# Kernel tuning notes

Measured on AMD Instinct MI355X. Metric: run time of the kernel, lower is better.

The kernel has to match this reference:

```python
import jax, jax.numpy as jnp
import numpy as np

N_NODES = 8192
N_EDGES = 16384
IN_CH = 32
HID = 64
OUT_CH = 2
EDGE_DIM = 4
N_LAYERS = 3
N_GRAPHS = 256
BN_EPS = 1e-5


def setup_inputs() -> dict:
    key = jax.random.key(0)
    ks = jax.random.split(key, 16)
    x = jax.random.normal(ks[0], (N_NODES, IN_CH), dtype=jnp.float32)
    edge_index = jax.random.randint(ks[1], (2, N_EDGES), 0, N_NODES, dtype=jnp.int32)
    edge_attr = jax.random.uniform(ks[2], (N_EDGES, EDGE_DIM), dtype=jnp.float32)
    batch = jnp.sort(jax.random.randint(ks[3], (N_NODES,), 0, N_GRAPHS, dtype=jnp.int32))
    s = 0.05
    params = {
        'lin_in_W': jax.random.normal(ks[4], (IN_CH, HID), jnp.float32) * s,
        'lin_in_b': jnp.zeros((HID,), jnp.float32),
        'edge_W': jax.random.normal(ks[5], (N_LAYERS, EDGE_DIM, HID * HID), jnp.float32) * s,
        'edge_b': jax.random.normal(ks[6], (N_LAYERS, HID * HID), jnp.float32) * s,
        'root_W': jax.random.normal(ks[7], (N_LAYERS, HID, HID), jnp.float32) * s,
        'conv_b': jnp.zeros((N_LAYERS, HID), jnp.float32),
        'bn_gamma': jnp.ones((N_LAYERS, HID), jnp.float32),
        'bn_beta': jnp.zeros((N_LAYERS, HID), jnp.float32),
        'bn_mean': jax.random.normal(ks[8], (N_LAYERS, HID), jnp.float32) * s,
        'bn_var': jax.random.uniform(ks[9], (N_LAYERS, HID), jnp.float32, 0.5, 1.5),
        'clf_W': jax.random.normal(ks[10], (HID, OUT_CH), jnp.float32) * s,
        'clf_b': jnp.zeros((OUT_CH,), jnp.float32),
    }
    return {'x': x, 'edge_index': edge_index, 'edge_attr': edge_attr, 'batch': batch, **params}


def reference(x, edge_index, edge_attr, batch, lin_in_W, lin_in_b, edge_W, edge_b,
              root_W, conv_b, bn_gamma, bn_beta, bn_mean, bn_var, clf_W, clf_b):
    # lin_in
    h = x @ lin_in_W + lin_in_b  # [N, H]
    src, dst = edge_index[0], edge_index[1]  # PyG: row0 = source j, row1 = target i
    for l in range(N_LAYERS):
        # edge network: per-edge weight matrix [E, H, H]
        W_e = (edge_attr @ edge_W[l] + edge_b[l]).reshape(N_EDGES, HID, HID)
        # message: gather x_j, per-edge matmul
        msg = jnp.einsum('eh,eho->eo', h[src], W_e)  # [E, H]
        # scatter-add aggregation at target nodes
        agg = jax.ops.segment_sum(msg, dst, num_segments=N_NODES)  # [N, H]
        # NNConv update: root transform + bias
        h = agg + h @ root_W[l] + conv_b[l]
        # BatchNorm1d (inference: running stats), then ReLU (dropout off in eval)
        h = (h - bn_mean[l]) * jax.lax.rsqrt(bn_var[l] + BN_EPS) * bn_gamma[l] + bn_beta[l]
        h = jax.nn.relu(h)
    # global_add_pool over graph ids
    pooled = jax.ops.segment_sum(h, batch, num_segments=N_GRAPHS)  # [G, H]
    return pooled @ clf_W + clf_b  # [G, OUT_CH]
```

## Files before the change

kernel.cpp:

```cpp
#include <hip/hip_runtime.h>
#include <hip/hip_bf16.h>

#define N_NODES 8192
#define N_EDGES 16384
#define IN_CH 32
#define HID 64
#define OUT_CH 2
#define EDGE_DIM 4
#define N_LAYERS 3
#define N_GRAPHS 256
#define BN_EPS 1e-5f
#define NT 512
#define NPB 32

__device__ __forceinline__ void ynet_phase(const float* __restrict__ hs,
                                           const float* __restrict__ eW,
                                           const float* __restrict__ eB,
                                           float4* __restrict__ y4,
                                           float* __restrict__ yb,
                                           int node0, int c, int g) {
    float acc[4][5];
#pragma unroll
    for (int j = 0; j < 4; ++j)
#pragma unroll
        for (int d = 0; d < 5; ++d) acc[j][d] = 0.f;

    const float4* h0v = (const float4*)(hs + (g * 4 + 0) * HID);
    const float4* h1v = (const float4*)(hs + (g * 4 + 1) * HID);
    const float4* h2v = (const float4*)(hs + (g * 4 + 2) * HID);
    const float4* h3v = (const float4*)(hs + (g * 4 + 3) * HID);

#pragma unroll 2
    for (int k4 = 0; k4 < HID / 4; ++k4) {
        float4 hv[4];
        hv[0] = h0v[k4]; hv[1] = h1v[k4]; hv[2] = h2v[k4]; hv[3] = h3v[k4];
        const float* hf = (const float*)hv;
#pragma unroll
        for (int kk = 0; kk < 4; ++kk) {
            int k = k4 * 4 + kk;
            float w0 = eW[0 * 4096 + k * 64 + c];
            float w1 = eW[1 * 4096 + k * 64 + c];
            float w2 = eW[2 * 4096 + k * 64 + c];
            float w3 = eW[3 * 4096 + k * 64 + c];
            float w4 = eB[k * 64 + c];
#pragma unroll
            for (int j = 0; j < 4; ++j) {
                float hk = hf[j * 4 + kk];
                acc[j][0] += hk * w0;
                acc[j][1] += hk * w1;
                acc[j][2] += hk * w2;
                acc[j][3] += hk * w3;
                acc[j][4] += hk * w4;
            }
        }
    }
#pragma unroll
    for (int j = 0; j < 4; ++j) {
        int n = node0 + g * 4 + j;
        y4[n * HID + c] = make_float4(acc[j][0], acc[j][1], acc[j][2], acc[j][3]);
        yb[n * HID + c] = acc[j][4];
    }
}

__global__ __launch_bounds__(NT) void k0_fused(
        const float* __restrict__ x,
        const float* __restrict__ Win, const float* __restrict__ bin,
        const float* __restrict__ eW0, const float* __restrict__ eB0,
        float* __restrict__ hA, float4* __restrict__ y4, float* __restrict__ yb,
        float* __restrict__ agg, float* __restrict__ pooled) {
    __shared__ float Wis[IN_CH * HID];
    __shared__ float xs[NPB * IN_CH];
    __shared__ float hs[NPB * HID];
    int t = threadIdx.x;
    int node0 = blockIdx.x * NPB;

    for (int i = t; i < NPB * HID; i += NT) agg[node0 * HID + i] = 0.f;
    if (t < 64) pooled[blockIdx.x * 64 + t] = 0.f;
    for (int i = t; i < IN_CH * HID; i += NT) Wis[i] = Win[i];
    for (int i = t; i < NPB * IN_CH; i += NT) xs[i] = x[node0 * IN_CH + i];
    __syncthreads();

    int c = t & 63, g = t >> 6;
    float b = bin[c];
    float a0 = b, a1 = b, a2 = b, a3 = b;
    const float* x0 = xs + (g * 4 + 0) * IN_CH;
    const float* x1 = xs + (g * 4 + 1) * IN_CH;
    const float* x2 = xs + (g * 4 + 2) * IN_CH;
    const float* x3 = xs + (g * 4 + 3) * IN_CH;
#pragma unroll
    for (int k = 0; k < IN_CH; ++k) {
        float wk = Wis[k * HID + c];
        a0 += x0[k] * wk; a1 += x1[k] * wk; a2 += x2[k] * wk; a3 += x3[k] * wk;
    }
    hs[(g * 4 + 0) * HID + c] = a0; hA[(node0 + g * 4 + 0) * HID + c] = a0;
    hs[(g * 4 + 1) * HID + c] = a1; hA[(node0 + g * 4 + 1) * HID + c] = a1;
    hs[(g * 4 + 2) * HID + c] = a2; hA[(node0 + g * 4 + 2) * HID + c] = a2;
    hs[(g * 4 + 3) * HID + c] = a3; hA[(node0 + g * 4 + 3) * HID + c] = a3;
    __syncthreads();

    ynet_phase(hs, eW0, eB0, y4, yb, node0, c, g);
}

__global__ __launch_bounds__(256) void edge_kernel(
        const float4* __restrict__ y4, const float* __restrict__ yb,
        const float* __restrict__ edge_attr, const int* __restrict__ edge_index,
        float* __restrict__ agg) {
    int e = blockIdx.x * 4 + (threadIdx.x >> 6);
    int lane = threadIdx.x & 63;
    int src = edge_index[e];
    int dst = edge_index[N_EDGES + e];
    float4 a = *(const float4*)(edge_attr + (size_t)e * 4);
    float4 yv = y4[(size_t)src * HID + lane];
    float m = a.x * yv.x + a.y * yv.y + a.z * yv.z + a.w * yv.w +
              yb[(size_t)src * HID + lane];
    atomicAdd(&agg[dst * HID + lane], m);
}

__global__ __launch_bounds__(NT) void k_upd_ynet(
        const float* __restrict__ h_in, float* __restrict__ agg,
        const float* __restrict__ rootW, const float* __restrict__ conv_b,
        const float* __restrict__ gam, const float* __restrict__ bet,
        const float* __restrict__ mu, const float* __restrict__ var,
        const float* __restrict__ eW_next, const float* __restrict__ eB_next,
        float* __restrict__ h_out, float4* __restrict__ y4, float* __restrict__ yb) {
    __shared__ float Ws[HID * HID];
    __shared__ float hsin[NPB * HID];
    __shared__ float hs[NPB * HID];
    int t = threadIdx.x;
    int node0 = blockIdx.x * NPB;
    for (int i = t; i < HID * HID; i += NT) Ws[i] = rootW[i];
    for (int i = t; i < NPB * HID; i += NT) hsin[i] = h_in[node0 * HID + i];
    __syncthreads();

    int c = t & 63, g = t >> 6;
    float scale = gam[c] * rsqrtf(var[c] + BN_EPS);
    float shift = bet[c] - mu[c] * scale;
    float cb = conv_b[c];

    float acc[4] = {0.f, 0.f, 0.f, 0.f};
    const float4* h0v = (const float4*)(hsin + (g * 4 + 0) * HID);
    const float4* h1v = (const float4*)(hsin + (g * 4 + 1) * HID);
    const float4* h2v = (const float4*)(hsin + (g * 4 + 2) * HID);
    const float4* h3v = (const float4*)(hsin + (g * 4 + 3) * HID);
#pragma unroll 4
    for (int k4 = 0; k4 < HID / 4; ++k4) {
        float4 hv[4];
        hv[0] = h0v[k4]; hv[1] = h1v[k4]; hv[2] = h2v[k4]; hv[3] = h3v[k4];
        const float* hf = (const float*)hv;
#pragma unroll
        for (int kk = 0; kk < 4; ++kk) {
            float wk = Ws[(k4 * 4 + kk) * 64 + c];
#pragma unroll
            for (int j = 0; j < 4; ++j) acc[j] += hf[j * 4 + kk] * wk;
        }
    }
#pragma unroll
    for (int j = 0; j < 4; ++j) {
        int node = node0 + g * 4 + j;
        float av = agg[node * HID + c];
        agg[node * HID + c] = 0.f;
        float v = fmaxf((av + acc[j] + cb) * scale + shift, 0.f);
        hs[(g * 4 + j) * HID + c] = v;
        h_out[node * HID + c] = v;
    }
    __syncthreads();

    ynet_phase(hs, eW_next, eB_next, y4, yb, node0, c, g);
}

__global__ __launch_bounds__(NT) void k_upd_pool(
        const float* __restrict__ h_in, float* __restrict__ agg,
        const float* __restrict__ rootW, const float* __restrict__ conv_b,
        const float* __restrict__ gam, const float* __restrict__ bet,
        const float* __restrict__ mu, const float* __restrict__ var,
        const int* __restrict__ batch, float* __restrict__ pooled) {
    __shared__ float Ws[HID * HID];
    __shared__ float hsin[NPB * HID];
    int t = threadIdx.x;
    int node0 = blockIdx.x * NPB;
    for (int i = t; i < HID * HID; i += NT) Ws[i] = rootW[i];
    for (int i = t; i < NPB * HID; i += NT) hsin[i] = h_in[node0 * HID + i];
    __syncthreads();

    int c = t & 63, g = t >> 6;
    float scale = gam[c] * rsqrtf(var[c] + BN_EPS);
    float shift = bet[c] - mu[c] * scale;
    float cb = conv_b[c];

    float acc[4] = {0.f, 0.f, 0.f, 0.f};
    const float4* h0v = (const float4*)(hsin + (g * 4 + 0) * HID);
    const float4* h1v = (const float4*)(hsin + (g * 4 + 1) * HID);
    const float4* h2v = (const float4*)(hsin + (g * 4 + 2) * HID);
    const float4* h3v = (const float4*)(hsin + (g * 4 + 3) * HID);
#pragma unroll 4
    for (int k4 = 0; k4 < HID / 4; ++k4) {
        float4 hv[4];
        hv[0] = h0v[k4]; hv[1] = h1v[k4]; hv[2] = h2v[k4]; hv[3] = h3v[k4];
        const float* hf = (const float*)hv;
#pragma unroll
        for (int kk = 0; kk < 4; ++kk) {
            float wk = Ws[(k4 * 4 + kk) * 64 + c];
#pragma unroll
            for (int j = 0; j < 4; ++j) acc[j] += hf[j * 4 + kk] * wk;
        }
    }
#pragma unroll
    for (int j = 0; j < 4; ++j) {
        int node = node0 + g * 4 + j;
        float av = agg[node * HID + c];
        agg[node * HID + c] = 0.f;
        float v = fmaxf((av + acc[j] + cb) * scale + shift, 0.f);
        atomicAdd(&pooled[batch[node] * HID + c], v);
    }
}

__global__ void clf_kernel(float* __restrict__ pooled,
                           const float* __restrict__ W,
                           const float* __restrict__ b,
                           float* __restrict__ out) {
    int gph = threadIdx.x;
    float acc0 = b[0], acc1 = b[1];
    float* pr = pooled + gph * HID;
#pragma unroll
    for (int k = 0; k < HID; ++k) {
        float p = pr[k];
        acc0 += p * W[k * 2 + 0];
        acc1 += p * W[k * 2 + 1];
    }
    out[gph * 2 + 0] = acc0;
    out[gph * 2 + 1] = acc1;
#pragma unroll
    for (int k = 0; k < HID; ++k) pr[k] = 0.f;
}

extern "C" void kernel_launch(void* const* d_in, const int* in_sizes, int n_in,
                              void* d_out, int out_size, void* d_ws, size_t ws_size,
                              hipStream_t stream) {
    const float* x         = (const float*)d_in[0];
    const int*   edge_index= (const int*)  d_in[1];
    const float* edge_attr = (const float*)d_in[2];
    const int*   batch     = (const int*)  d_in[3];
    const float* lin_in_W  = (const float*)d_in[4];
    const float* lin_in_b  = (const float*)d_in[5];
    const float* edge_W    = (const float*)d_in[6];
    const float* edge_b    = (const float*)d_in[7];
    const float* root_W    = (const float*)d_in[8];
    const float* conv_b    = (const float*)d_in[9];
    const float* bn_gamma  = (const float*)d_in[10];
    const float* bn_beta   = (const float*)d_in[11];
    const float* bn_mean   = (const float*)d_in[12];
    const float* bn_var    = (const float*)d_in[13];
    const float* clf_W     = (const float*)d_in[14];
    const float* clf_b     = (const float*)d_in[15];
    float* out = (float*)d_out;

    char* ws = (char*)d_ws;
    float*  hA     = (float*) (ws);
    float*  hB     = (float*) (ws + (size_t)2 * 1024 * 1024);
    float*  agg    = (float*) (ws + (size_t)4 * 1024 * 1024);
    float*  yb     = (float*) (ws + (size_t)6 * 1024 * 1024);
    float*  pooled = (float*) (ws + (size_t)8 * 1024 * 1024);
    float4* y4     = (float4*)(ws + (size_t)9 * 1024 * 1024);

    k0_fused<<<N_NODES / NPB, NT, 0, stream>>>(
        x, lin_in_W, lin_in_b, edge_W, edge_b, hA, y4, yb, agg, pooled);

    edge_kernel<<<N_EDGES / 4, 256, 0, stream>>>(y4, yb, edge_attr, edge_index, agg);

    k_upd_ynet<<<N_NODES / NPB, NT, 0, stream>>>(
        hA, agg, root_W, conv_b, bn_gamma, bn_beta, bn_mean, bn_var,
        edge_W + (size_t)1 * EDGE_DIM * HID * HID, edge_b + (size_t)1 * HID * HID,
        hB, y4, yb);

    edge_kernel<<<N_EDGES / 4, 256, 0, stream>>>(y4, yb, edge_attr, edge_index, agg);

    k_upd_ynet<<<N_NODES / NPB, NT, 0, stream>>>(
        hB, agg, root_W + (size_t)1 * HID * HID, conv_b + (size_t)1 * HID,
        bn_gamma + HID, bn_beta + HID, bn_mean + HID, bn_var + HID,
        edge_W + (size_t)2 * EDGE_DIM * HID * HID, edge_b + (size_t)2 * HID * HID,
        hA, y4, yb);

    edge_kernel<<<N_EDGES / 4, 256, 0, stream>>>(y4, yb, edge_attr, edge_index, agg);

    k_upd_pool<<<N_NODES / NPB, NT, 0, stream>>>(
        hA, agg, root_W + (size_t)2 * HID * HID, conv_b + (size_t)2 * HID,
        bn_gamma + 2 * HID, bn_beta + 2 * HID, bn_mean + 2 * HID, bn_var + 2 * HID,
        batch, pooled);

    clf_kernel<<<1, 256, 0, stream>>>(pooled, clf_W, clf_b, out);
}
```

Baseline: 89.86 us.

## Fuse all layers into one cooperative kernel with per-block edge gather

```diff
diff --git a/kernel.cpp b/kernel.cpp
--- a/kernel.cpp
+++ b/kernel.cpp
@@ -1,5 +1,7 @@
 #include <hip/hip_runtime.h>
-#include <hip/hip_bf16.h>
+#include <hip/hip_cooperative_groups.h>
+
+namespace cg = cooperative_groups;
 
 #define N_NODES 8192
 #define N_EDGES 16384
@@ -10,8 +12,23 @@
 #define N_LAYERS 3
 #define N_GRAPHS 256
 #define BN_EPS 1e-5f
+
+#define NBLK 256
 #define NT 512
 #define NPB 32
+#define CAP 24
+
+#define FB_NT 512
+#define FB_NPB 32
+
+struct KP {
+    const float* x; const int* edge_index; const float* edge_attr; const int* batch;
+    const float* lin_in_W; const float* lin_in_b; const float* edge_W; const float* edge_b;
+    const float* root_W; const float* conv_b; const float* bn_gamma; const float* bn_beta;
+    const float* bn_mean; const float* bn_var; const float* clf_W; const float* clf_b;
+    float* out;
+    float* y4A; float* ybA; float* y4B; float* ybB; float* pooled;
+};
 
 __device__ __forceinline__ void ynet_phase(const float* __restrict__ hs,
                                            const float* __restrict__ eW,
@@ -56,28 +73,159 @@
     }
 #pragma unroll
     for (int j = 0; j < 4; ++j) {
-        int n = node0 + g * 4 + j;
+        size_t n = node0 + g * 4 + j;
         y4[n * HID + c] = make_float4(acc[j][0], acc[j][1], acc[j][2], acc[j][3]);
         yb[n * HID + c] = acc[j][4];
     }
 }
 
-__global__ __launch_bounds__(NT) void k0_fused(
+__global__ __launch_bounds__(NT, 2) void mega(KP P) {
+    cg::grid_group grid = cg::this_grid();
+
+    __shared__ float  hs[NPB * HID];
+    __shared__ float  smem[HID * HID];
+    __shared__ int    cntL[NPB];
+    __shared__ int    esrcL[NPB * CAP];
+    __shared__ float4 ea4L[NPB * CAP];
+
+    const int t = threadIdx.x;
+    const int b = blockIdx.x;
+    const int node0 = b * NPB;
+    const int c = t & 63, g = t >> 6;
+
+    {
+        int gi = b * NT + t;
+        if (gi < N_GRAPHS * HID) P.pooled[gi] = 0.f;
+    }
+    if (t < NPB) cntL[t] = 0;
+    float* Wis = smem;
+    float* xs  = smem + IN_CH * HID;
+    for (int i = t; i < IN_CH * HID; i += NT) Wis[i] = P.lin_in_W[i];
+    for (int i = t; i < NPB * IN_CH; i += NT) xs[i] = P.x[node0 * IN_CH + i];
+    __syncthreads();
+
+    for (int e = t; e < N_EDGES; e += NT) {
+        int dst = P.edge_index[N_EDGES + e];
+        int local = dst - node0;
+        if ((unsigned)local < NPB) {
+            int slot = atomicAdd(&cntL[local], 1);
+            if (slot < CAP) {
+                esrcL[local * CAP + slot] = P.edge_index[e];
+                ea4L[local * CAP + slot] = *(const float4*)(P.edge_attr + 4 * (size_t)e);
+            }
+        }
+    }
+
+    {
+        float bb = P.lin_in_b[c];
+        float a0 = bb, a1 = bb, a2 = bb, a3 = bb;
+        const float* x0 = xs + (g * 4 + 0) * IN_CH;
+        const float* x1 = xs + (g * 4 + 1) * IN_CH;
+        const float* x2 = xs + (g * 4 + 2) * IN_CH;
+        const float* x3 = xs + (g * 4 + 3) * IN_CH;
+#pragma unroll
+        for (int k = 0; k < IN_CH; ++k) {
+            float wk = Wis[k * HID + c];
+            a0 += x0[k] * wk; a1 += x1[k] * wk; a2 += x2[k] * wk; a3 += x3[k] * wk;
+        }
+        hs[(g * 4 + 0) * HID + c] = a0;
+        hs[(g * 4 + 1) * HID + c] = a1;
+        hs[(g * 4 + 2) * HID + c] = a2;
+        hs[(g * 4 + 3) * HID + c] = a3;
+    }
+
+    ynet_phase(hs, P.edge_W, P.edge_b, (float4*)P.y4A, P.ybA, node0, c, g);
+
+    grid.sync();
+
+    const float4* ycur4 = (const float4*)P.y4A;
+    const float*  ycurb = P.ybA;
+    float4* ynxt4 = (float4*)P.y4B;
+    float*  ynxtb = P.ybB;
+
+    for (int l = 0; l < N_LAYERS; ++l) {
+        for (int i = t; i < HID * HID; i += NT)
+            smem[i] = P.root_W[(size_t)l * HID * HID + i];
+        __syncthreads();
+
+        float scale = P.bn_gamma[l * HID + c] * rsqrtf(P.bn_var[l * HID + c] + BN_EPS);
+        float shift = P.bn_beta[l * HID + c] - P.bn_mean[l * HID + c] * scale;
+        float cb = P.conv_b[l * HID + c];
+
+        float hnew[4];
+#pragma unroll
+        for (int j = 0; j < 4; ++j) {
+            int ln = g * 4 + j;
+            float m = 0.f;
+            int d = cntL[ln]; d = (d > CAP) ? CAP : d;
+            for (int s = 0; s < d; ++s) {
+                int src = esrcL[ln * CAP + s];
+                float4 a = ea4L[ln * CAP + s];
+                float4 yv = ycur4[(size_t)src * HID + c];
+                m += a.x * yv.x + a.y * yv.y + a.z * yv.z + a.w * yv.w +
+                     ycurb[(size_t)src * HID + c];
+            }
+            float acc = 0.f;
+            const float4* hv = (const float4*)(hs + ln * HID);
+#pragma unroll
+            for (int k4 = 0; k4 < HID / 4; ++k4) {
+                float4 h4 = hv[k4];
+                const float* hf = (const float*)&h4;
+#pragma unroll
+                for (int kk = 0; kk < 4; ++kk)
+                    acc += hf[kk] * smem[(k4 * 4 + kk) * HID + c];
+            }
+            hnew[j] = fmaxf((m + acc + cb) * scale + shift, 0.f);
+        }
+#pragma unroll
+        for (int j = 0; j < 4; ++j) hs[(g * 4 + j) * HID + c] = hnew[j];
+
+        if (l < N_LAYERS - 1) {
+            ynet_phase(hs, P.edge_W + (size_t)(l + 1) * EDGE_DIM * HID * HID,
+                       P.edge_b + (size_t)(l + 1) * HID * HID, ynxt4, ynxtb, node0, c, g);
+        } else {
+#pragma unroll
+            for (int j = 0; j < 4; ++j) {
+                int n = node0 + g * 4 + j;
+                atomicAdd(&P.pooled[P.batch[n] * HID + c], hnew[j]);
+            }
+        }
+        const float4* t4 = ycur4; ycur4 = (const float4*)ynxt4; ynxt4 = (float4*)t4;
+        const float*  tb = ycurb; ycurb = ynxtb; ynxtb = (float*)tb;
+
+        grid.sync();
+    }
+
+    if (b == 0 && t < N_GRAPHS) {
+        float acc0 = P.clf_b[0], acc1 = P.clf_b[1];
+        const float* pr = P.pooled + t * HID;
+#pragma unroll
+        for (int k = 0; k < HID; ++k) {
+            float p = pr[k];
+            acc0 += p * P.clf_W[k * 2 + 0];
+            acc1 += p * P.clf_W[k * 2 + 1];
+        }
+        P.out[t * 2 + 0] = acc0;
+        P.out[t * 2 + 1] = acc1;
+    }
+}
+
+__global__ __launch_bounds__(FB_NT) void fb_k0(
         const float* __restrict__ x,
         const float* __restrict__ Win, const float* __restrict__ bin,
         const float* __restrict__ eW0, const float* __restrict__ eB0,
         float* __restrict__ hA, float4* __restrict__ y4, float* __restrict__ yb,
         float* __restrict__ agg, float* __restrict__ pooled) {
     __shared__ float Wis[IN_CH * HID];
-    __shared__ float xs[NPB * IN_CH];
-    __shared__ float hs[NPB * HID];
+    __shared__ float xs[FB_NPB * IN_CH];
+    __shared__ float hs[FB_NPB * HID];
     int t = threadIdx.x;
-    int node0 = blockIdx.x * NPB;
-
-    for (int i = t; i < NPB * HID; i += NT) agg[node0 * HID + i] = 0.f;
+    int node0 = blockIdx.x * FB_NPB;
+
+    for (int i = t; i < FB_NPB * HID; i += FB_NT) agg[node0 * HID + i] = 0.f;
     if (t < 64) pooled[blockIdx.x * 64 + t] = 0.f;
-    for (int i = t; i < IN_CH * HID; i += NT) Wis[i] = Win[i];
-    for (int i = t; i < NPB * IN_CH; i += NT) xs[i] = x[node0 * IN_CH + i];
+    for (int i = t; i < IN_CH * HID; i += FB_NT) Wis[i] = Win[i];
+    for (int i = t; i < FB_NPB * IN_CH; i += FB_NT) xs[i] = x[node0 * IN_CH + i];
     __syncthreads();
 
     int c = t & 63, g = t >> 6;
@@ -101,7 +249,7 @@
     ynet_phase(hs, eW0, eB0, y4, yb, node0, c, g);
 }
 
-__global__ __launch_bounds__(256) void edge_kernel(
+__global__ __launch_bounds__(256) void fb_edge(
         const float4* __restrict__ y4, const float* __restrict__ yb,
         const float* __restrict__ edge_attr, const int* __restrict__ edge_index,
         float* __restrict__ agg) {
@@ -116,7 +264,7 @@
     atomicAdd(&agg[dst * HID + lane], m);
 }
 
-__global__ __launch_bounds__(NT) void k_upd_ynet(
+__global__ __launch_bounds__(FB_NT) void fb_upd(
         const float* __restrict__ h_in, float* __restrict__ agg,
         const float* __restrict__ rootW, const float* __restrict__ conv_b,
         const float* __restrict__ gam, const float* __restrict__ bet,
@@ -124,12 +272,12 @@
         const float* __restrict__ eW_next, const float* __restrict__ eB_next,
         float* __restrict__ h_out, float4* __restrict__ y4, float* __restrict__ yb) {
     __shared__ float Ws[HID * HID];
-    __shared__ float hsin[NPB * HID];
-    __shared__ float hs[NPB * HID];
+    __shared__ float hsin[FB_NPB * HID];
+    __shared__ float hs[FB_NPB * HID];
     int t = threadIdx.x;
-    int node0 = blockIdx.x * NPB;
-    for (int i = t; i < HID * HID; i += NT) Ws[i] = rootW[i];
-    for (int i = t; i < NPB * HID; i += NT) hsin[i] = h_in[node0 * HID + i];
+    int node0 = blockIdx.x * FB_NPB;
+    for (int i = t; i < HID * HID; i += FB_NT) Ws[i] = rootW[i];
+    for (int i = t; i < FB_NPB * HID; i += FB_NT) hsin[i] = h_in[node0 * HID + i];
     __syncthreads();
 
     int c = t & 63, g = t >> 6;
@@ -168,18 +316,18 @@
     ynet_phase(hs, eW_next, eB_next, y4, yb, node0, c, g);
 }
 
-__global__ __launch_bounds__(NT) void k_upd_pool(
+__global__ __launch_bounds__(FB_NT) void fb_upd_pool(
         const float* __restrict__ h_in, float* __restrict__ agg,
         const float* __restrict__ rootW, const float* __restrict__ conv_b,
         const float* __restrict__ gam, const float* __restrict__ bet,
         const float* __restrict__ mu, const float* __restrict__ var,
         const int* __restrict__ batch, float* __restrict__ pooled) {
     __shared__ float Ws[HID * HID];
-    __shared__ float hsin[NPB * HID];
+    __shared__ float hsin[FB_NPB * HID];
     int t = threadIdx.x;
-    int node0 = blockIdx.x * NPB;
-    for (int i = t; i < HID * HID; i += NT) Ws[i] = rootW[i];
-    for (int i = t; i < NPB * HID; i += NT) hsin[i] = h_in[node0 * HID + i];
+    int node0 = blockIdx.x * FB_NPB;
+    for (int i = t; i < HID * HID; i += FB_NT) Ws[i] = rootW[i];
+    for (int i = t; i < FB_NPB * HID; i += FB_NT) hsin[i] = h_in[node0 * HID + i];
     __syncthreads();
 
     int c = t & 63, g = t >> 6;
@@ -214,10 +362,10 @@
     }
 }
 
-__global__ void clf_kernel(float* __restrict__ pooled,
-                           const float* __restrict__ W,
-                           const float* __restrict__ b,
-                           float* __restrict__ out) {
+__global__ void fb_clf(float* __restrict__ pooled,
+                       const float* __restrict__ W,
+                       const float* __restrict__ b,
+                       float* __restrict__ out) {
     int gph = threadIdx.x;
     float acc0 = b[0], acc1 = b[1];
     float* pr = pooled + gph * HID;
@@ -236,56 +384,83 @@
 extern "C" void kernel_launch(void* const* d_in, const int* in_sizes, int n_in,
                               void* d_out, int out_size, void* d_ws, size_t ws_size,
                               hipStream_t stream) {
-    const float* x         = (const float*)d_in[0];
-    const int*   edge_index= (const int*)  d_in[1];
-    const float* edge_attr = (const float*)d_in[2];
-    const int*   batch     = (const int*)  d_in[3];
-    const float* lin_in_W  = (const float*)d_in[4];
-    const float* lin_in_b  = (const float*)d_in[5];
-    const float* edge_W    = (const float*)d_in[6];
-    const float* edge_b    = (const float*)d_in[7];
-    const float* root_W    = (const float*)d_in[8];
-    const float* conv_b    = (const float*)d_in[9];
-    const float* bn_gamma  = (const float*)d_in[10];
-    const float* bn_beta   = (const float*)d_in[11];
-    const float* bn_mean   = (const float*)d_in[12];
-    const float* bn_var    = (const float*)d_in[13];
-    const float* clf_W     = (const float*)d_in[14];
-    const float* clf_b     = (const float*)d_in[15];
-    float* out = (float*)d_out;
-
     char* ws = (char*)d_ws;
-    float*  hA     = (float*) (ws);
-    float*  hB     = (float*) (ws + (size_t)2 * 1024 * 1024);
-    float*  agg    = (float*) (ws + (size_t)4 * 1024 * 1024);
-    float*  yb     = (float*) (ws + (size_t)6 * 1024 * 1024);
-    float*  pooled = (float*) (ws + (size_t)8 * 1024 * 1024);
-    float4* y4     = (float4*)(ws + (size_t)9 * 1024 * 1024);
-
-    k0_fused<<<N_NODES / NPB, NT, 0, stream>>>(
-        x, lin_in_W, lin_in_b, edge_W, edge_b, hA, y4, yb, agg, pooled);
-
-    edge_kernel<<<N_EDGES / 4, 256, 0, stream>>>(y4, yb, edge_attr, edge_index, agg);
-
-    k_upd_ynet<<<N_NODES / NPB, NT, 0, stream>>>(
-        hA, agg, root_W, conv_b, bn_gamma, bn_beta, bn_mean, bn_var,
-        edge_W + (size_t)1 * EDGE_DIM * HID * HID, edge_b + (size_t)1 * HID * HID,
-        hB, y4, yb);
-
-    edge_kernel<<<N_EDGES / 4, 256, 0, stream>>>(y4, yb, edge_attr, edge_index, agg);
-
-    k_upd_ynet<<<N_NODES / NPB, NT, 0, stream>>>(
-        hB, agg, root_W + (size_t)1 * HID * HID, conv_b + (size_t)1 * HID,
-        bn_gamma + HID, bn_beta + HID, bn_mean + HID, bn_var + HID,
-        edge_W + (size_t)2 * EDGE_DIM * HID * HID, edge_b + (size_t)2 * HID * HID,
-        hA, y4, yb);
-
-    edge_kernel<<<N_EDGES / 4, 256, 0, stream>>>(y4, yb, edge_attr, edge_index, agg);
-
-    k_upd_pool<<<N_NODES / NPB, NT, 0, stream>>>(
-        hA, agg, root_W + (size_t)2 * HID * HID, conv_b + (size_t)2 * HID,
-        bn_gamma + 2 * HID, bn_beta + 2 * HID, bn_mean + 2 * HID, bn_var + 2 * HID,
-        batch, pooled);
-
-    clf_kernel<<<1, 256, 0, stream>>>(pooled, clf_W, clf_b, out);
-}
+    KP p;
+    p.x          = (const float*)d_in[0];
+    p.edge_index = (const int*)  d_in[1];
+    p.edge_attr  = (const float*)d_in[2];
+    p.batch      = (const int*)  d_in[3];
+    p.lin_in_W   = (const float*)d_in[4];
+    p.lin_in_b   = (const float*)d_in[5];
+    p.edge_W     = (const float*)d_in[6];
+    p.edge_b     = (const float*)d_in[7];
+    p.root_W     = (const float*)d_in[8];
+    p.conv_b     = (const float*)d_in[9];
+    p.bn_gamma   = (const float*)d_in[10];
+    p.bn_beta    = (const float*)d_in[11];
+    p.bn_mean    = (const float*)d_in[12];
+    p.bn_var     = (const float*)d_in[13];
+    p.clf_W      = (const float*)d_in[14];
+    p.clf_b      = (const float*)d_in[15];
+    p.out        = (float*)d_out;
+    p.y4A   = (float*)(ws);
+    p.y4B   = (float*)(ws + (size_t) 8 * 1024 * 1024);
+    p.ybA   = (float*)(ws + (size_t)16 * 1024 * 1024);
+    p.ybB   = (float*)(ws + (size_t)18 * 1024 * 1024);
+    p.pooled= (float*)(ws + (size_t)20 * 1024 * 1024);
+
+    float*  hA  = (float*) (ws + (size_t)21 * 1024 * 1024);
+    float*  hB  = (float*) (ws + (size_t)23 * 1024 * 1024);
+    float*  agg = (float*) (ws + (size_t)25 * 1024 * 1024);
+    float*  yb  = p.ybA;
+    float4* y4  = (float4*)p.y4A;
+    float*  pooled = p.pooled;
+
+    int dev = 0;
+    hipGetDevice(&dev);
+    int coopAttr = 0, numCU = 0, maxB = 0;
+    hipDeviceGetAttribute(&coopAttr, hipDeviceAttributeCooperativeLaunch, dev);
+    hipDeviceGetAttribute(&numCU, hipDeviceAttributeMultiprocessorCount, dev);
+    hipError_t oe = hipOccupancyMaxActiveBlocksPerMultiprocessor(
+        &maxB, (const void*)mega, NT, 0);
+
+    hipError_t lerr = hipErrorUnknown;
+    if (coopAttr && oe == hipSuccess && maxB >= 1 && maxB * numCU >= NBLK) {
+        void* args[] = { &p };
+        lerr = hipLaunchCooperativeKernel((const void*)mega, dim3(NBLK), dim3(NT),
+                                          args, 0, stream);
+    }
+    if (lerr != hipSuccess) {
+        const float* edge_W = p.edge_W;
+        const float* edge_b = p.edge_b;
+        const float* root_W = p.root_W;
+        const float* conv_b = p.conv_b;
+
+        fb_k0<<<N_NODES / FB_NPB, FB_NT, 0, stream>>>(
+            p.x, p.lin_in_W, p.lin_in_b, edge_W, edge_b, hA, y4, yb, agg, pooled);
+
+        fb_edge<<<N_EDGES / 4, 256, 0, stream>>>(y4, yb, p.edge_attr, p.edge_index, agg);
+
+        fb_upd<<<N_NODES / FB_NPB, FB_NT, 0, stream>>>(
+            hA, agg, root_W, conv_b, p.bn_gamma, p.bn_beta, p.bn_mean, p.bn_var,
+            edge_W + (size_t)1 * EDGE_DIM * HID * HID, edge_b + (size_t)1 * HID * HID,
+            hB, y4, yb);
+
+        fb_edge<<<N_EDGES / 4, 256, 0, stream>>>(y4, yb, p.edge_attr, p.edge_index, agg);
+
+        fb_upd<<<N_NODES / FB_NPB, FB_NT, 0, stream>>>(
+            hB, agg, root_W + (size_t)1 * HID * HID, conv_b + (size_t)1 * HID,
+            p.bn_gamma + HID, p.bn_beta + HID, p.bn_mean + HID, p.bn_var + HID,
+            edge_W + (size_t)2 * EDGE_DIM * HID * HID, edge_b + (size_t)2 * HID * HID,
+            hA, y4, yb);
+
+        fb_edge<<<N_EDGES / 4, 256, 0, stream>>>(y4, yb, p.edge_attr, p.edge_index, agg);
+
+        fb_upd_pool<<<N_NODES / FB_NPB, FB_NT, 0, stream>>>(
+            hA, agg, root_W + (size_t)2 * HID * HID, conv_b + (size_t)2 * HID,
+            p.bn_gamma + 2 * HID, p.bn_beta + 2 * HID, p.bn_mean + 2 * HID,
+            p.bn_var + 2 * HID, p.batch, pooled);
+
+        fb_clf<<<1, 256, 0, stream>>>(pooled, p.clf_W, p.clf_b, p.out);
+    }
+}
```

Result: no change. 90.15 us (+0.3%).

## Replace atomic edge scatter with per-node bucketed gather fused into layer kernels

Applied to the files above, without the earlier changes.

```diff
diff --git a/kernel.cpp b/kernel.cpp
--- a/kernel.cpp
+++ b/kernel.cpp
@@ -10,8 +10,11 @@
 #define N_LAYERS 3
 #define N_GRAPHS 256
 #define BN_EPS 1e-5f
-#define NT 512
-#define NPB 32
+
+#define NBLK 512
+#define NT 256
+#define NPB 16
+#define CAP 24
 
 __device__ __forceinline__ void ynet_phase(const float* __restrict__ hs,
                                            const float* __restrict__ eW,
@@ -56,171 +59,152 @@
     }
 #pragma unroll
     for (int j = 0; j < 4; ++j) {
-        int n = node0 + g * 4 + j;
+        size_t n = node0 + g * 4 + j;
         y4[n * HID + c] = make_float4(acc[j][0], acc[j][1], acc[j][2], acc[j][3]);
         yb[n * HID + c] = acc[j][4];
     }
 }
 
-__global__ __launch_bounds__(NT) void k0_fused(
+__global__ __launch_bounds__(NT) void k0(
         const float* __restrict__ x,
         const float* __restrict__ Win, const float* __restrict__ bin,
         const float* __restrict__ eW0, const float* __restrict__ eB0,
-        float* __restrict__ hA, float4* __restrict__ y4, float* __restrict__ yb,
-        float* __restrict__ agg, float* __restrict__ pooled) {
+        const int* __restrict__ edge_index, const float* __restrict__ edge_attr,
+        float* __restrict__ hG, float4* __restrict__ y4, float* __restrict__ yb,
+        int* __restrict__ bcnt, int* __restrict__ bsrc, float4* __restrict__ bea,
+        float* __restrict__ pooled) {
     __shared__ float Wis[IN_CH * HID];
     __shared__ float xs[NPB * IN_CH];
     __shared__ float hs[NPB * HID];
-    int t = threadIdx.x;
-    int node0 = blockIdx.x * NPB;
-
-    for (int i = t; i < NPB * HID; i += NT) agg[node0 * HID + i] = 0.f;
-    if (t < 64) pooled[blockIdx.x * 64 + t] = 0.f;
+    __shared__ int   cntL[NPB];
+    const int t = threadIdx.x, b = blockIdx.x, node0 = b * NPB;
+    const int c = t & 63, g = t >> 6;
+
+    int gi = b * NT + t;
+    if (gi < N_GRAPHS * HID) pooled[gi] = 0.f;
+    if (t < NPB) cntL[t] = 0;
     for (int i = t; i < IN_CH * HID; i += NT) Wis[i] = Win[i];
     for (int i = t; i < NPB * IN_CH; i += NT) xs[i] = x[node0 * IN_CH + i];
     __syncthreads();
 
-    int c = t & 63, g = t >> 6;
-    float b = bin[c];
-    float a0 = b, a1 = b, a2 = b, a3 = b;
-    const float* x0 = xs + (g * 4 + 0) * IN_CH;
-    const float* x1 = xs + (g * 4 + 1) * IN_CH;
-    const float* x2 = xs + (g * 4 + 2) * IN_CH;
-    const float* x3 = xs + (g * 4 + 3) * IN_CH;
-#pragma unroll
-    for (int k = 0; k < IN_CH; ++k) {
-        float wk = Wis[k * HID + c];
-        a0 += x0[k] * wk; a1 += x1[k] * wk; a2 += x2[k] * wk; a3 += x3[k] * wk;
-    }
-    hs[(g * 4 + 0) * HID + c] = a0; hA[(node0 + g * 4 + 0) * HID + c] = a0;
-    hs[(g * 4 + 1) * HID + c] = a1; hA[(node0 + g * 4 + 1) * HID + c] = a1;
-    hs[(g * 4 + 2) * HID + c] = a2; hA[(node0 + g * 4 + 2) * HID + c] = a2;
-    hs[(g * 4 + 3) * HID + c] = a3; hA[(node0 + g * 4 + 3) * HID + c] = a3;
+    const int4* dst4 = (const int4*)(edge_index + N_EDGES);
+    for (int e4 = t; e4 < N_EDGES / 4; e4 += NT) {
+        int4 d4 = dst4[e4];
+        int ds[4] = {d4.x, d4.y, d4.z, d4.w};
+#pragma unroll
+        for (int q = 0; q < 4; ++q) {
+            int local = ds[q] - node0;
+            if ((unsigned)local < NPB) {
+                int e = e4 * 4 + q;
+                int slot = atomicAdd(&cntL[local], 1);
+                if (slot < CAP) {
+                    bsrc[(node0 + local) * CAP + slot] = edge_index[e];
+                    bea[(node0 + local) * CAP + slot] =
+                        *(const float4*)(edge_attr + 4 * (size_t)e);
+                }
+            }
+        }
+    }
     __syncthreads();
+    if (t < NPB) bcnt[node0 + t] = min(cntL[t], CAP);
+
+    {
+        float bb = bin[c];
+        float a0 = bb, a1 = bb, a2 = bb, a3 = bb;
+        const float* x0 = xs + (g * 4 + 0) * IN_CH;
+        const float* x1 = xs + (g * 4 + 1) * IN_CH;
+        const float* x2 = xs + (g * 4 + 2) * IN_CH;
+        const float* x3 = xs + (g * 4 + 3) * IN_CH;
+#pragma unroll
+        for (int k = 0; k < IN_CH; ++k) {
+            float wk = Wis[k * HID + c];
+            a0 += x0[k] * wk; a1 += x1[k] * wk; a2 += x2[k] * wk; a3 += x3[k] * wk;
+        }
+        hs[(g * 4 + 0) * HID + c] = a0; hG[(node0 + g * 4 + 0) * HID + c] = a0;
+        hs[(g * 4 + 1) * HID + c] = a1; hG[(node0 + g * 4 + 1) * HID + c] = a1;
+        hs[(g * 4 + 2) * HID + c] = a2; hG[(node0 + g * 4 + 2) * HID + c] = a2;
+        hs[(g * 4 + 3) * HID + c] = a3; hG[(node0 + g * 4 + 3) * HID + c] = a3;
+    }
 
     ynet_phase(hs, eW0, eB0, y4, yb, node0, c, g);
 }
 
-__global__ __launch_bounds__(256) void edge_kernel(
-        const float4* __restrict__ y4, const float* __restrict__ yb,
-        const float* __restrict__ edge_attr, const int* __restrict__ edge_index,
-        float* __restrict__ agg) {
-    int e = blockIdx.x * 4 + (threadIdx.x >> 6);
-    int lane = threadIdx.x & 63;
-    int src = edge_index[e];
-    int dst = edge_index[N_EDGES + e];
-    float4 a = *(const float4*)(edge_attr + (size_t)e * 4);
-    float4 yv = y4[(size_t)src * HID + lane];
-    float m = a.x * yv.x + a.y * yv.y + a.z * yv.z + a.w * yv.w +
-              yb[(size_t)src * HID + lane];
-    atomicAdd(&agg[dst * HID + lane], m);
-}
-
-__global__ __launch_bounds__(NT) void k_upd_ynet(
-        const float* __restrict__ h_in, float* __restrict__ agg,
+template <int LAST>
+__global__ __launch_bounds__(NT) void klayer(
+        float* __restrict__ hG,
+        const float4* __restrict__ ycur4, const float* __restrict__ ycurb,
+        float4* __restrict__ ynxt4, float* __restrict__ ynxtb,
         const float* __restrict__ rootW, const float* __restrict__ conv_b,
         const float* __restrict__ gam, const float* __restrict__ bet,
         const float* __restrict__ mu, const float* __restrict__ var,
         const float* __restrict__ eW_next, const float* __restrict__ eB_next,
-        float* __restrict__ h_out, float4* __restrict__ y4, float* __restrict__ yb) {
+        const int* __restrict__ bcnt, const int* __restrict__ bsrc,
+        const float4* __restrict__ bea,
+        const int* __restrict__ batch, float* __restrict__ pooled) {
     __shared__ float Ws[HID * HID];
-    __shared__ float hsin[NPB * HID];
     __shared__ float hs[NPB * HID];
-    int t = threadIdx.x;
-    int node0 = blockIdx.x * NPB;
+    __shared__ int   cntS[NPB];
+    const int t = threadIdx.x, b = blockIdx.x, node0 = b * NPB;
+    const int c = t & 63, g = t >> 6;
+
     for (int i = t; i < HID * HID; i += NT) Ws[i] = rootW[i];
-    for (int i = t; i < NPB * HID; i += NT) hsin[i] = h_in[node0 * HID + i];
+    for (int i = t; i < NPB * HID; i += NT) hs[i] = hG[node0 * HID + i];
+    if (t < NPB) cntS[t] = bcnt[node0 + t];
     __syncthreads();
 
-    int c = t & 63, g = t >> 6;
     float scale = gam[c] * rsqrtf(var[c] + BN_EPS);
     float shift = bet[c] - mu[c] * scale;
     float cb = conv_b[c];
 
-    float acc[4] = {0.f, 0.f, 0.f, 0.f};
-    const float4* h0v = (const float4*)(hsin + (g * 4 + 0) * HID);
-    const float4* h1v = (const float4*)(hsin + (g * 4 + 1) * HID);
-    const float4* h2v = (const float4*)(hsin + (g * 4 + 2) * HID);
-    const float4* h3v = (const float4*)(hsin + (g * 4 + 3) * HID);
-#pragma unroll 4
-    for (int k4 = 0; k4 < HID / 4; ++k4) {
-        float4 hv[4];
-        hv[0] = h0v[k4]; hv[1] = h1v[k4]; hv[2] = h2v[k4]; hv[3] = h3v[k4];
-        const float* hf = (const float*)hv;
-#pragma unroll
-        for (int kk = 0; kk < 4; ++kk) {
-            float wk = Ws[(k4 * 4 + kk) * 64 + c];
-#pragma unroll
-            for (int j = 0; j < 4; ++j) acc[j] += hf[j * 4 + kk] * wk;
-        }
-    }
+    float hnew[4];
 #pragma unroll
     for (int j = 0; j < 4; ++j) {
-        int node = node0 + g * 4 + j;
-        float av = agg[node * HID + c];
-        agg[node * HID + c] = 0.f;
-        float v = fmaxf((av + acc[j] + cb) * scale + shift, 0.f);
-        hs[(g * 4 + j) * HID + c] = v;
-        h_out[node * HID + c] = v;
-    }
-    __syncthreads();
-
-    ynet_phase(hs, eW_next, eB_next, y4, yb, node0, c, g);
-}
-
-__global__ __launch_bounds__(NT) void k_upd_pool(
-        const float* __restrict__ h_in, float* __restrict__ agg,
-        const float* __restrict__ rootW, const float* __restrict__ conv_b,
-        const float* __restrict__ gam, const float* __restrict__ bet,
-        const float* __restrict__ mu, const float* __restrict__ var,
-        const int* __restrict__ batch, float* __restrict__ pooled) {
-    __shared__ float Ws[HID * HID];
-    __shared__ float hsin[NPB * HID];
-    int t = threadIdx.x;
-    int node0 = blockIdx.x * NPB;
-    for (int i = t; i < HID * HID; i += NT) Ws[i] = rootW[i];
-    for (int i = t; i < NPB * HID; i += NT) hsin[i] = h_in[node0 * HID + i];
-    __syncthreads();
-
-    int c = t & 63, g = t >> 6;
-    float scale = gam[c] * rsqrtf(var[c] + BN_EPS);
-    float shift = bet[c] - mu[c] * scale;
-    float cb = conv_b[c];
-
-    float acc[4] = {0.f, 0.f, 0.f, 0.f};
-    const float4* h0v = (const float4*)(hsin + (g * 4 + 0) * HID);
-    const float4* h1v = (const float4*)(hsin + (g * 4 + 1) * HID);
-    const float4* h2v = (const float4*)(hsin + (g * 4 + 2) * HID);
-    const float4* h3v = (const float4*)(hsin + (g * 4 + 3) * HID);
-#pragma unroll 4
-    for (int k4 = 0; k4 < HID / 4; ++k4) {
-        float4 hv[4];
-        hv[0] = h0v[k4]; hv[1] = h1v[k4]; hv[2] = h2v[k4]; hv[3] = h3v[k4];
-        const float* hf = (const float*)hv;
-#pragma unroll
-        for (int kk = 0; kk < 4; ++kk) {
-            float wk = Ws[(k4 * 4 + kk) * 64 + c];
-#pragma unroll
-            for (int j = 0; j < 4; ++j) acc[j] += hf[j * 4 + kk] * wk;
-        }
-    }
-#pragma unroll
-    for (int j = 0; j < 4; ++j) {
-        int node = node0 + g * 4 + j;
-        float av = agg[node * HID + c];
-        agg[node * HID + c] = 0.f;
-        float v = fmaxf((av + acc[j] + cb) * scale + shift, 0.f);
-        atomicAdd(&pooled[batch[node] * HID + c], v);
-    }
-}
-
-__global__ void clf_kernel(float* __restrict__ pooled,
+        int ln = g * 4 + j;
+        int node = node0 + ln;
+        float m = 0.f;
+        int d = cntS[ln];
+        for (int s = 0; s < d; ++s) {
+            int src = bsrc[node * CAP + s];
+            float4 a = bea[node * CAP + s];
+            float4 yv = ycur4[(size_t)src * HID + c];
+            m += a.x * yv.x + a.y * yv.y + a.z * yv.z + a.w * yv.w +
+                 ycurb[(size_t)src * HID + c];
+        }
+        float acc = 0.f;
+        const float4* hv = (const float4*)(hs + ln * HID);
+#pragma unroll
+        for (int k4 = 0; k4 < HID / 4; ++k4) {
+            float4 h4 = hv[k4];
+            acc += h4.x * Ws[(k4 * 4 + 0) * 64 + c] +
+                   h4.y * Ws[(k4 * 4 + 1) * 64 + c] +
+                   h4.z * Ws[(k4 * 4 + 2) * 64 + c] +
+                   h4.w * Ws[(k4 * 4 + 3) * 64 + c];
+        }
+        hnew[j] = fmaxf((m + acc + cb) * scale + shift, 0.f);
+    }
+#pragma unroll
+    for (int j = 0; j < 4; ++j) hs[(g * 4 + j) * HID + c] = hnew[j];
+
+    if (!LAST) {
+#pragma unroll
+        for (int j = 0; j < 4; ++j) hG[(node0 + g * 4 + j) * HID + c] = hnew[j];
+        ynet_phase(hs, eW_next, eB_next, ynxt4, ynxtb, node0, c, g);
+    } else {
+#pragma unroll
+        for (int j = 0; j < 4; ++j) {
+            int n = node0 + g * 4 + j;
+            atomicAdd(&pooled[batch[n] * HID + c], hnew[j]);
+        }
+    }
+}
+
+__global__ void clf_kernel(const float* __restrict__ pooled,
                            const float* __restrict__ W,
                            const float* __restrict__ b,
                            float* __restrict__ out) {
     int gph = threadIdx.x;
     float acc0 = b[0], acc1 = b[1];
-    float* pr = pooled + gph * HID;
+    const float* pr = pooled + gph * HID;
 #pragma unroll
     for (int k = 0; k < HID; ++k) {
         float p = pr[k];
@@ -229,8 +213,6 @@
     }
     out[gph * 2 + 0] = acc0;
     out[gph * 2 + 1] = acc1;
-#pragma unroll
-    for (int k = 0; k < HID; ++k) pr[k] = 0.f;
 }
 
 extern "C" void kernel_launch(void* const* d_in, const int* in_sizes, int n_in,
@@ -255,37 +237,39 @@
     float* out = (float*)d_out;
 
     char* ws = (char*)d_ws;
-    float*  hA     = (float*) (ws);
-    float*  hB     = (float*) (ws + (size_t)2 * 1024 * 1024);
-    float*  agg    = (float*) (ws + (size_t)4 * 1024 * 1024);
-    float*  yb     = (float*) (ws + (size_t)6 * 1024 * 1024);
-    float*  pooled = (float*) (ws + (size_t)8 * 1024 * 1024);
-    float4* y4     = (float4*)(ws + (size_t)9 * 1024 * 1024);
-
-    k0_fused<<<N_NODES / NPB, NT, 0, stream>>>(
-        x, lin_in_W, lin_in_b, edge_W, edge_b, hA, y4, yb, agg, pooled);
-
-    edge_kernel<<<N_EDGES / 4, 256, 0, stream>>>(y4, yb, edge_attr, edge_index, agg);
-
-    k_upd_ynet<<<N_NODES / NPB, NT, 0, stream>>>(
-        hA, agg, root_W, conv_b, bn_gamma, bn_beta, bn_mean, bn_var,
+    float4* y4A    = (float4*)(ws);
+    float4* y4B    = (float4*)(ws + (size_t) 8 * 1024 * 1024);
+    float*  ybA    = (float*) (ws + (size_t)16 * 1024 * 1024);
+    float*  ybB    = (float*) (ws + (size_t)18 * 1024 * 1024);
+    float*  pooled = (float*) (ws + (size_t)20 * 1024 * 1024);
+    float*  hG     = (float*) (ws + (size_t)21 * 1024 * 1024);
+    int*    bcnt   = (int*)   (ws + (size_t)23 * 1024 * 1024);
+    int*    bsrc   = (int*)   (ws + (size_t)24 * 1024 * 1024);
+    float4* bea    = (float4*)(ws + (size_t)25 * 1024 * 1024);
+
+    k0<<<NBLK, NT, 0, stream>>>(x, lin_in_W, lin_in_b, edge_W, edge_b,
+                                edge_index, edge_attr, hG, y4A, ybA,
+                                bcnt, bsrc, bea, pooled);
+
+    klayer<0><<<NBLK, NT, 0, stream>>>(
+        hG, y4A, ybA, y4B, ybB,
+        root_W, conv_b, bn_gamma, bn_beta, bn_mean, bn_var,
         edge_W + (size_t)1 * EDGE_DIM * HID * HID, edge_b + (size_t)1 * HID * HID,
-        hB, y4, yb);
-
-    edge_kernel<<<N_EDGES / 4, 256, 0, stream>>>(y4, yb, edge_attr, edge_index, agg);
-
-    k_upd_ynet<<<N_NODES / NPB, NT, 0, stream>>>(
-        hB, agg, root_W + (size_t)1 * HID * HID, conv_b + (size_t)1 * HID,
+        bcnt, bsrc, bea, batch, pooled);
+
+    klayer<0><<<NBLK, NT, 0, stream>>>(
+        hG, y4B, ybB, y4A, ybA,
+        root_W + (size_t)1 * HID * HID, conv_b + (size_t)1 * HID,
         bn_gamma + HID, bn_beta + HID, bn_mean + HID, bn_var + HID,
         edge_W + (size_t)2 * EDGE_DIM * HID * HID, edge_b + (size_t)2 * HID * HID,
-        hA, y4, yb);
-
-    edge_kernel<<<N_EDGES / 4, 256, 0, stream>>>(y4, yb, edge_attr, edge_index, agg);
-
-    k_upd_pool<<<N_NODES / NPB, NT, 0, stream>>>(
-        hA, agg, root_W + (size_t)2 * HID * HID, conv_b + (size_t)2 * HID,
+        bcnt, bsrc, bea, batch, pooled);
+
+    klayer<1><<<NBLK, NT, 0, stream>>>(
+        hG, y4A, ybA, y4B, ybB,
+        root_W + (size_t)2 * HID * HID, conv_b + (size_t)2 * HID,
         bn_gamma + 2 * HID, bn_beta + 2 * HID, bn_mean + 2 * HID, bn_var + 2 * HID,
-        batch, pooled);
+        edge_W, edge_b,
+        bcnt, bsrc, bea, batch, pooled);
 
     clf_kernel<<<1, 256, 0, stream>>>(pooled, clf_W, clf_b, out);
 }
```

Result: slower. 118.8 us (+32.3%).
